# Kernel optimization log

Hardware: AMD Instinct MI355X
Metric: run time of the kernel (lower is better)

The kernel has to match this reference:

```python
import jax, jax.numpy as jnp
import numpy as np

# CLEVR-scale dims
B, N, DF, DE, DV, H, NC, QV, L = 128, 36, 512, 256, 512, 256, 28, 2000, 5


def _lin(key, fan_in, fan_out):
    k1, _ = jax.random.split(key)
    w = jax.random.normal(k1, (fan_in, fan_out), jnp.float32) * np.sqrt(2.0 / fan_in)  # kaiming
    b = jnp.zeros((fan_out,), jnp.float32)
    return w, b


def setup_inputs() -> dict:
    key = jax.random.key(0)
    ks = jax.random.split(key, 12)
    node_feats = jax.random.normal(ks[0], (B, N, DF), jnp.float32)
    edge_feats = jax.random.normal(ks[1], (B, N, N, DE), jnp.float32)
    programs = jax.random.randint(ks[2], (B, L), 0, 10)
    program_inputs = jax.random.randint(ks[3], (B, L), 0, QV)
    W_n1, b_n1 = _lin(ks[4], DF, H)
    W_n2, b_n2 = _lin(ks[5], H, DV)
    W_e1, b_e1 = _lin(ks[6], DE, H)
    W_e2, b_e2 = _lin(ks[7], H, DV)
    W_q, b_q = _lin(ks[8], DV, DV)
    W_c1, b_c1 = _lin(ks[9], DV, H)
    W_c2, b_c2 = _lin(ks[10], H, NC)
    word_emb = jax.random.normal(ks[11], (QV, DV), jnp.float32) / np.sqrt(DV)
    return dict(node_feats=node_feats, edge_feats=edge_feats,
                W_n1=W_n1, b_n1=b_n1, W_n2=W_n2, b_n2=b_n2,
                W_e1=W_e1, b_e1=b_e1, W_e2=W_e2, b_e2=b_e2,
                W_q=W_q, b_q=b_q, W_c1=W_c1, b_c1=b_c1,
                W_c2=W_c2, b_c2=b_c2, word_emb=word_emb,
                programs=programs, program_inputs=program_inputs)


def _mlp(x, W1, b1, W2, b2):
    return jax.nn.relu(x @ W1 + b1) @ W2 + b2


def reference(node_feats, edge_feats, W_n1, b_n1, W_n2, b_n2,
              W_e1, b_e1, W_e2, b_e2, W_q, b_q,
              W_c1, b_c1, W_c2, b_c2, word_emb,
              programs, program_inputs):
    # Fixed representative program (executed in reverse order like the torch code):
    # scene -> filter -> relate -> filter -> query -> classifier
    del programs
    scale = 1.0 / np.sqrt(DV)
    nf = _mlp(node_feats, W_n1, b_n1, W_n2, b_n2)      # [B,N,DV]  map_node_feat_to_v
    ef = _mlp(edge_feats, W_e1, b_e1, W_e2, b_e2)      # [B,N,N,DV] map_edge_feat_to_v
    q = word_emb[program_inputs]                        # [B,L,DV]  word_embedding lookup
    # scene: attention of ones over nodes
    attn = jnp.ones(nf.shape[:2], nf.dtype)             # [B,N]
    # filter (AttentionModule): gate node attention by query-node similarity
    attn = attn * jax.nn.sigmoid(jnp.einsum('bnd,bd->bn', nf, q[:, 3]) * scale)
    # relate (RelateModule): transfer attention along query-weighted edges
    weit = jax.nn.sigmoid(jnp.einsum('bijd,bd->bij', ef, q[:, 2]) * scale)  # [B,N,N]
    attn = jnp.clip(jnp.einsum('bi,bij->bj', attn, weit), 0.0, 1.0)
    # filter again
    attn = attn * jax.nn.sigmoid(jnp.einsum('bnd,bd->bn', nf, q[:, 1]) * scale)
    # query (QueryModule): attention-pooled node feature gated by query, projected
    attn_n = attn / (attn.sum(-1, keepdims=True) + 1e-8)
    pooled = jnp.einsum('bn,bnd->bd', attn_n, nf)        # [B,DV]
    out = jax.nn.relu((pooled * q[:, 0]) @ W_q + b_q)    # [B,DV]
    # classifier
    return jax.nn.relu(out @ W_c1 + b_c1) @ W_c2 + b_c2  # [B,NC]
```

## Files before the change

### kernel.cpp

```cpp
#include <hip/hip_runtime.h>
#include <math.h>

#define BB 128
#define NN 36
#define DF 512
#define DE 256
#define DV 512
#define HH 256
#define NCC 28
#define LQ 5
#define NE 1296
#define SCALE 0.04419417382415922f

#define EDGE_BLOCKS 3456
#define NODE_BLOCKS 288

typedef __bf16 bf16_8 __attribute__((ext_vector_type(8)));
typedef float  f32_4  __attribute__((ext_vector_type(4)));

__device__ __forceinline__ float sigmoidf_(float x){ return 1.0f/(1.0f + expf(-x)); }
__device__ __forceinline__ float reluf_(float x){ return x > 0.f ? x : 0.f; }

__device__ __forceinline__ bf16_8 cvt8(f32_4 f0, f32_4 f1){
    bf16_8 v;
    #pragma unroll
    for (int i=0;i<4;i++){ v[i] = (__bf16)f0[i]; v[i+4] = (__bf16)f1[i]; }
    return v;
}
__device__ __forceinline__ void split8(f32_4 f0, f32_4 f1, bf16_8& h, bf16_8& l){
    #pragma unroll
    for (int i=0;i<4;i++){
        __bf16 hi = (__bf16)f0[i];
        h[i] = hi; l[i] = (__bf16)(f0[i] - (float)hi);
        __bf16 hi2 = (__bf16)f1[i];
        h[i+4] = hi2; l[i+4] = (__bf16)(f1[i] - (float)hi2);
    }
}

__device__ __forceinline__ void async_copy16(const float* g, float* lds_base){
    __builtin_amdgcn_global_load_lds(
        (const __attribute__((address_space(1))) void*)g,
        (__attribute__((address_space(3))) void*)lds_base, 16, 0, 0);
}

#define XROW 516
#define EROW 260

__global__ __launch_bounds__(256) void k_setup(
    const float* __restrict__ W_n1, const float* __restrict__ W_n2,
    const float* __restrict__ W_q,  const float* __restrict__ W_c1,
    const float* __restrict__ W_e1, const float* __restrict__ W_c2,
    const float* __restrict__ word_emb, const int* __restrict__ program_inputs,
    const float* __restrict__ W_e2, const float* __restrict__ b_e2,
    __bf16* __restrict__ Pn1h, __bf16* __restrict__ Pn1l,
    __bf16* __restrict__ Pn2h, __bf16* __restrict__ Pn2l,
    __bf16* __restrict__ Pqh,  __bf16* __restrict__ Pql,
    __bf16* __restrict__ Pc1h, __bf16* __restrict__ Pc1l,
    __bf16* __restrict__ Peh,
    __bf16* __restrict__ Pc2h, __bf16* __restrict__ Pc2l,
    float* __restrict__ qws, float* __restrict__ ve, float* __restrict__ se)
{
    int bid = blockIdx.x;
    if (bid < 356){
        const float* W; __bf16 *Ph, *Pl; int N, base, realN;
        if (bid < 64)       { W=W_n1; Ph=Pn1h; Pl=Pn1l; N=256; base=0;   realN=256; }
        else if (bid < 128) { W=W_n2; Ph=Pn2h; Pl=Pn2l; N=512; base=64;  realN=512; }
        else if (bid < 256) { W=W_q;  Ph=Pqh;  Pl=Pql;  N=512; base=128; realN=512; }
        else if (bid < 320) { W=W_c1; Ph=Pc1h; Pl=Pc1l; N=256; base=256; realN=256; }
        else if (bid < 352) { W=W_e1; Ph=Peh;  Pl=nullptr; N=256; base=320; realN=256; }
        else                { W=W_c2; Ph=Pc2h; Pl=Pc2l; N=32;  base=352; realN=28;  }
        int g = (bid-base)*256 + threadIdx.x;
        int lane = g & 63, slot = g >> 6;
        int NT = N >> 4;
        int nt = slot % NT, kt = slot / NT;
        int krow = kt*32 + (lane>>4)*8, ncol = nt*16 + (lane&15);
        #pragma unroll
        for (int j=0;j<8;j++){
            float w = (ncol < realN) ? W[(size_t)(krow+j)*realN + ncol] : 0.f;
            __bf16 hi = (__bf16)w;
            Ph[(size_t)g*8+j] = hi;
            if (Pl) Pl[(size_t)g*8+j] = (__bf16)(w - (float)hi);
        }
    } else {
        int b = bid - 356, t = threadIdx.x, wv = t>>6, lane = t&63;
        int idx[4];
        #pragma unroll
        for (int k=0;k<4;k++) idx[k] = program_inputs[b*LQ + k];
        #pragma unroll
        for (int k=0;k<4;k++){
            qws[((size_t)(b*4+k))*DV + t]       = word_emb[(size_t)idx[k]*DV + t];
            qws[((size_t)(b*4+k))*DV + t + 256] = word_emb[(size_t)idx[k]*DV + t + 256];
        }
        const float* q2p = word_emb + (size_t)idx[2]*DV + lane*8;
        f32_4 qa = *(const f32_4*)q2p, qb = *(const f32_4*)(q2p+4);
        for (int i=0;i<64;i++){
            int h = wv*64 + i;
            const float* wr = W_e2 + (size_t)h*DV + lane*8;
            f32_4 a = *(const f32_4*)wr, c = *(const f32_4*)(wr+4);
            float p = a[0]*qa[0] + a[1]*qa[1] + a[2]*qa[2] + a[3]*qa[3]
                    + c[0]*qb[0] + c[1]*qb[1] + c[2]*qb[2] + c[3]*qb[3];
            #pragma unroll
            for (int off=32; off; off>>=1) p += __shfl_xor(p, off, 64);
            if (lane==0) ve[b*HH + h] = p;
        }
        float pp = b_e2[t]*word_emb[(size_t)idx[2]*DV + t]
                 + b_e2[t+256]*word_emb[(size_t)idx[2]*DV + t + 256];
        __shared__ float red[4];
        #pragma unroll
        for (int off=32; off; off>>=1) pp += __shfl_down(pp, off, 64);
        if ((t&63)==0) red[t>>6] = pp;
        __syncthreads();
        if (t==0) se[b] = red[0]+red[1]+red[2]+red[3];
    }
}

__device__ __forceinline__ void edge_body(
    int bx, char* smem,
    const float* __restrict__ E, const __bf16* __restrict__ Wp,
    const float* __restrict__ b_e1, const float* __restrict__ ve,
    const float* __restrict__ se, float* __restrict__ weit)
{
    float* es  = (float*)smem;
    float* red = (float*)(smem + 48*EROW*4);
    int b = bx / 27, tile = bx % 27;
    int e0 = tile*48;
    int t = threadIdx.x, wv = t>>6, lane = t&63;
    int m = lane&15, kc = lane>>4;
    const float* Eb = E + ((size_t)b*NE + e0)*DE;

    #pragma unroll
    for (int r=0;r<12;r++){
        int row = wv*12 + r;
        async_copy16(Eb + (size_t)row*DE + lane*4, &es[row*EROW]);
    }
    __syncthreads();

    f32_4 zero = {0.f,0.f,0.f,0.f};
    f32_4 acc[3][4];
    #pragma unroll
    for (int mt=0;mt<3;mt++)
        #pragma unroll
        for (int nt=0;nt<4;nt++) acc[mt][nt] = zero;

    for (int kt=0; kt<8; kt++){
        bf16_8 af[3];
        #pragma unroll
        for (int mt=0;mt<3;mt++){
            const float* ap = &es[(mt*16 + m)*EROW + kt*32 + kc*8];
            af[mt] = cvt8(*(const f32_4*)ap, *(const f32_4*)(ap+4));
        }
        #pragma unroll
        for (int nt=0;nt<4;nt++){
            bf16_8 bfrag = *(const bf16_8*)(Wp + ((size_t)(kt*16 + (wv*4+nt))*64 + lane)*8);
            #pragma unroll
            for (int mt=0;mt<3;mt++)
                acc[mt][nt] = __builtin_amdgcn_mfma_f32_16x16x32_bf16(af[mt], bfrag, acc[mt][nt], 0,0,0);
        }
    }

    float ves[4], be[4];
    #pragma unroll
    for (int nt=0;nt<4;nt++){
        int n = wv*64 + nt*16 + m;
        ves[nt] = ve[b*HH + n];
        be[nt]  = b_e1[n];
    }
    float part[3][4];
    #pragma unroll
    for (int mt=0;mt<3;mt++)
        #pragma unroll
        for (int r=0;r<4;r++){
            float s = 0.f;
            #pragma unroll
            for (int nt=0;nt<4;nt++)
                s = fmaf(reluf_(acc[mt][nt][r] + be[nt]), ves[nt], s);
            part[mt][r] = s;
        }
    #pragma unroll
    for (int off=1; off<16; off<<=1)
        #pragma unroll
        for (int mt=0;mt<3;mt++)
            #pragma unroll
            for (int r=0;r<4;r++)
                part[mt][r] += __shfl_xor(part[mt][r], off, 64);
    if (m==0){
        int g = lane>>4;
        #pragma unroll
        for (int mt=0;mt<3;mt++)
            #pragma unroll
            for (int r=0;r<4;r++)
                red[wv*48 + mt*16 + g*4 + r] = part[mt][r];
    }
    __syncthreads();
    if (t < 48){
        float logit = red[0*48+t]+red[1*48+t]+red[2*48+t]+red[3*48+t] + se[b];
        weit[(size_t)b*NE + e0 + t] = sigmoidf_(logit * SCALE);
    }
}

__device__ __forceinline__ void node_body(
    int nb, char* smem,
    const float* __restrict__ X,
    const __bf16* __restrict__ W1h, const __bf16* __restrict__ W1l,
    const float* __restrict__ b1,
    const __bf16* __restrict__ W2h, const __bf16* __restrict__ W2l,
    const float* __restrict__ b2,
    float* __restrict__ nf)
{
    float* xs  = (float*)smem;
    __bf16* hh = (__bf16*)(smem + 33024);
    __bf16* hl = (__bf16*)(smem + 41216);
    int r0 = nb*16, t = threadIdx.x, wv = t>>6, lane = t&63;
    int m = lane&15, kc = lane>>4;
    int q = lane>>4, c = lane&15;

    #pragma unroll
    for (int r=0;r<4;r++){
        int row = wv*4 + r;
        const float* src = X + (size_t)(r0+row)*DF + lane*4;
        async_copy16(src,       &xs[row*XROW]);
        async_copy16(src + 256, &xs[row*XROW + 256]);
    }
    __syncthreads();

    f32_4 zero = {0.f,0.f,0.f,0.f};
    f32_4 acc1[4];
    #pragma unroll
    for (int nt=0;nt<4;nt++) acc1[nt] = zero;
    for (int kt=0; kt<16; kt++){
        const float* ap = &xs[m*XROW + kt*32 + kc*8];
        f32_4 f0 = *(const f32_4*)ap;
        f32_4 f1 = *(const f32_4*)(ap+4);
        bf16_8 ah, al;
        split8(f0, f1, ah, al);
        #pragma unroll
        for (int nt=0;nt<4;nt++){
            size_t bo = ((size_t)(kt*16 + wv*4+nt)*64 + lane)*8;
            bf16_8 bh = *(const bf16_8*)(W1h + bo);
            bf16_8 bl = *(const bf16_8*)(W1l + bo);
            acc1[nt] = __builtin_amdgcn_mfma_f32_16x16x32_bf16(ah, bh, acc1[nt], 0,0,0);
            acc1[nt] = __builtin_amdgcn_mfma_f32_16x16x32_bf16(al, bh, acc1[nt], 0,0,0);
            acc1[nt] = __builtin_amdgcn_mfma_f32_16x16x32_bf16(ah, bl, acc1[nt], 0,0,0);
        }
    }
    #pragma unroll
    for (int nt=0;nt<4;nt++){
        int col = wv*64 + nt*16 + c;
        float bias = b1[col];
        int kt2 = col>>5, j2 = col&7;
        int lbase = ((col&31)>>3)*16;
        #pragma unroll
        for (int r=0;r<4;r++){
            int row = q*4 + r;
            float v = reluf_(acc1[nt][r] + bias);
            __bf16 hi = (__bf16)v;
            int off = (kt2*64 + lbase + row)*8 + j2;
            hh[off] = hi;
            hl[off] = (__bf16)(v - (float)hi);
        }
    }
    __syncthreads();

    f32_4 acc2[8];
    #pragma unroll
    for (int nt=0;nt<8;nt++) acc2[nt] = zero;
    for (int kt=0; kt<8; kt++){
        bf16_8 ah = *(const bf16_8*)&hh[(kt*64+lane)*8];
        bf16_8 al = *(const bf16_8*)&hl[(kt*64+lane)*8];
        #pragma unroll
        for (int nt=0;nt<8;nt++){
            size_t bo = ((size_t)(kt*32 + wv*8+nt)*64 + lane)*8;
            bf16_8 bh = *(const bf16_8*)(W2h + bo);
            bf16_8 bl = *(const bf16_8*)(W2l + bo);
            acc2[nt] = __builtin_amdgcn_mfma_f32_16x16x32_bf16(ah, bh, acc2[nt], 0,0,0);
            acc2[nt] = __builtin_amdgcn_mfma_f32_16x16x32_bf16(al, bh, acc2[nt], 0,0,0);
            acc2[nt] = __builtin_amdgcn_mfma_f32_16x16x32_bf16(ah, bl, acc2[nt], 0,0,0);
        }
    }
    #pragma unroll
    for (int nt=0;nt<8;nt++){
        int col = wv*128 + nt*16 + c;
        float bias = b2[col];
        #pragma unroll
        for (int r=0;r<4;r++){
            int row = q*4 + r;
            nf[(size_t)(r0+row)*DV + col] = acc2[nt][r] + bias;
        }
    }
}

__global__ __launch_bounds__(256) void k_main(
    const float* __restrict__ E, const __bf16* __restrict__ Wp,
    const float* __restrict__ b_e1, const float* __restrict__ ve,
    const float* __restrict__ se, float* __restrict__ weit,
    const float* __restrict__ X,
    const __bf16* __restrict__ W1h, const __bf16* __restrict__ W1l,
    const float* __restrict__ b1,
    const __bf16* __restrict__ W2h, const __bf16* __restrict__ W2l,
    const float* __restrict__ b2,
    float* __restrict__ nf)
{
    __shared__ __align__(16) char smem[50688];
    int bx = blockIdx.x;
    if (bx < EDGE_BLOCKS)
        edge_body(bx, smem, E, Wp, b_e1, ve, se, weit);
    else
        node_body(bx - EDGE_BLOCKS, smem, X, W1h, W1l, b1, W2h, W2l, b2, nf);
}

__global__ __launch_bounds__(256) void k_attn(
    const float* __restrict__ nf, const float* __restrict__ qws,
    const float* __restrict__ weit, float* __restrict__ xws)
{
    int b = blockIdx.x, t = threadIdx.x;
    int wv = t>>6, lane = t&63;
    __shared__ float a1[NN], a2[NN], a3[NN];
    __shared__ float denom;
    const float* nfb = nf + (size_t)b*NN*DV;
    const float* q0 = qws + ((size_t)(b*4+0))*DV;
    const float* q1 = qws + ((size_t)(b*4+1))*DV;
    const float* q3 = qws + ((size_t)(b*4+3))*DV;

    #pragma unroll
    for (int i=wv; i<NN; i+=4){
        const float* row = nfb + (size_t)i*DV + lane*8;
        const float* qq  = q3 + lane*8;
        f32_4 x0 = *(const f32_4*)row, x1 = *(const f32_4*)(row+4);
        f32_4 y0 = *(const f32_4*)qq,  y1 = *(const f32_4*)(qq+4);
        float p = x0[0]*y0[0] + x0[1]*y0[1] + x0[2]*y0[2] + x0[3]*y0[3]
                + x1[0]*y1[0] + x1[1]*y1[1] + x1[2]*y1[2] + x1[3]*y1[3];
        #pragma unroll
        for (int off=32; off; off>>=1) p += __shfl_xor(p, off, 64);
        if (lane==0) a1[i] = sigmoidf_(p*SCALE);
    }
    __syncthreads();
    if (t < NN){
        const float* wrow = weit + (size_t)b*NE;
        float s = 0.f;
        #pragma unroll
        for (int i=0;i<NN;i++) s = fmaf(a1[i], wrow[i*NN + t], s);
        a2[t] = fminf(fmaxf(s, 0.f), 1.f);
    }
    __syncthreads();
    #pragma unroll
    for (int i=wv; i<NN; i+=4){
        const float* row = nfb + (size_t)i*DV + lane*8;
        const float* qq  = q1 + lane*8;
        f32_4 x0 = *(const f32_4*)row, x1 = *(const f32_4*)(row+4);
        f32_4 y0 = *(const f32_4*)qq,  y1 = *(const f32_4*)(qq+4);
        float p = x0[0]*y0[0] + x0[1]*y0[1] + x0[2]*y0[2] + x0[3]*y0[3]
                + x1[0]*y1[0] + x1[1]*y1[1] + x1[2]*y1[2] + x1[3]*y1[3];
        #pragma unroll
        for (int off=32; off; off>>=1) p += __shfl_xor(p, off, 64);
        if (lane==0) a3[i] = a2[i]*sigmoidf_(p*SCALE);
    }
    __syncthreads();
    if (t==0){
        float s = 0.f;
        for (int i=0;i<NN;i++) s += a3[i];
        denom = 1.f/(s + 1e-8f);
    }
    __syncthreads();
    float p0=0.f, p1=0.f;
    #pragma unroll
    for (int i=0;i<NN;i++){
        float a = a3[i]*denom;
        p0 = fmaf(a, nfb[(size_t)i*DV + t], p0);
        p1 = fmaf(a, nfb[(size_t)i*DV + t + 256], p1);
    }
    xws[(size_t)b*DV + t]       = p0*q0[t];
    xws[(size_t)b*DV + t + 256] = p1*q0[t+256];
}

__global__ __launch_bounds__(256) void k_head(
    const float* __restrict__ xws,
    const __bf16* __restrict__ Wqh, const __bf16* __restrict__ Wql,
    const float* __restrict__ b_q,
    const __bf16* __restrict__ Wc1h, const __bf16* __restrict__ Wc1l,
    const float* __restrict__ b_c1,
    const __bf16* __restrict__ Pc2h, const __bf16* __restrict__ Pc2l,
    const float* __restrict__ b_c2,
    float* __restrict__ out)
{
    __shared__ __align__(16) char smem[49408];
    float* xs   = (float*)smem;
    __bf16* oh  = (__bf16*)smem;
    __bf16* ol  = (__bf16*)(smem + 16384);
    __bf16* hfh = (__bf16*)(smem + 33024);
    __bf16* hfl = (__bf16*)(smem + 41216);

    int r0 = blockIdx.x*16, t = threadIdx.x, wv = t>>6, lane = t&63;
    int m = lane&15, kc = lane>>4;
    int q = lane>>4, c = lane&15;
    f32_4 zero = {0.f,0.f,0.f,0.f};

    #pragma unroll
    for (int r=0;r<4;r++){
        int row = wv*4 + r;
        const float* src = xws + (size_t)(r0+row)*DV + lane*4;
        async_copy16(src,       &xs[row*XROW]);
        async_copy16(src + 256, &xs[row*XROW + 256]);
    }
    __syncthreads();

    f32_4 acc[8];
    #pragma unroll
    for (int nt=0;nt<8;nt++) acc[nt] = zero;
    for (int kt=0; kt<16; kt++){
        const float* ap = &xs[m*XROW + kt*32 + kc*8];
        f32_4 f0 = *(const f32_4*)ap;
        f32_4 f1 = *(const f32_4*)(ap+4);
        bf16_8 ah, al;
        split8(f0, f1, ah, al);
        #pragma unroll
        for (int nt=0;nt<8;nt++){
            size_t bo = ((size_t)(kt*32 + wv*8+nt)*64 + lane)*8;
            bf16_8 bh = *(const bf16_8*)(Wqh + bo);
            bf16_8 bl = *(const bf16_8*)(Wql + bo);
            acc[nt] = __builtin_amdgcn_mfma_f32_16x16x32_bf16(ah, bh, acc[nt], 0,0,0);
            acc[nt] = __builtin_amdgcn_mfma_f32_16x16x32_bf16(al, bh, acc[nt], 0,0,0);
            acc[nt] = __builtin_amdgcn_mfma_f32_16x16x32_bf16(ah, bl, acc[nt], 0,0,0);
        }
    }
    __syncthreads();
    #pragma unroll
    for (int nt=0;nt<8;nt++){
        int col = wv*128 + nt*16 + c;
        float bias = b_q[col];
        int kt2 = col>>5, j2 = col&7;
        int lbase = ((col&31)>>3)*16;
        #pragma unroll
        for (int r=0;r<4;r++){
            int row = q*4 + r;
            float v = reluf_(acc[nt][r] + bias);
            __bf16 hi = (__bf16)v;
            int off = (kt2*64 + lbase + row)*8 + j2;
            oh[off] = hi;
            ol[off] = (__bf16)(v - (float)hi);
        }
    }
    __syncthreads();

    f32_4 acc2[4];
    #pragma unroll
    for (int nt=0;nt<4;nt++) acc2[nt] = zero;
    for (int kt=0; kt<16; kt++){
        bf16_8 ah = *(const bf16_8*)&oh[(kt*64+lane)*8];
        bf16_8 al = *(const bf16_8*)&ol[(kt*64+lane)*8];
        #pragma unroll
        for (int nt=0;nt<4;nt++){
            size_t bo = ((size_t)(kt*16 + wv*4+nt)*64 + lane)*8;
            bf16_8 bh = *(const bf16_8*)(Wc1h + bo);
            bf16_8 bl = *(const bf16_8*)(Wc1l + bo);
            acc2[nt] = __builtin_amdgcn_mfma_f32_16x16x32_bf16(ah, bh, acc2[nt], 0,0,0);
            acc2[nt] = __builtin_amdgcn_mfma_f32_16x16x32_bf16(al, bh, acc2[nt], 0,0,0);
            acc2[nt] = __builtin_amdgcn_mfma_f32_16x16x32_bf16(ah, bl, acc2[nt], 0,0,0);
        }
    }
    #pragma unroll
    for (int nt=0;nt<4;nt++){
        int col = wv*64 + nt*16 + c;
        float bias = b_c1[col];
        int kt2 = col>>5, j2 = col&7;
        int lbase = ((col&31)>>3)*16;
        #pragma unroll
        for (int r=0;r<4;r++){
            int row = q*4 + r;
            float v = reluf_(acc2[nt][r] + bias);
            __bf16 hi = (__bf16)v;
            int off = (kt2*64 + lbase + row)*8 + j2;
            hfh[off] = hi;
            hfl[off] = (__bf16)(v - (float)hi);
        }
    }
    __syncthreads();

    if (wv < 2){
        f32_4 acc3 = zero;
        for (int kt=0; kt<8; kt++){
            bf16_8 ah = *(const bf16_8*)&hfh[(kt*64+lane)*8];
            bf16_8 al = *(const bf16_8*)&hfl[(kt*64+lane)*8];
            size_t bo = ((size_t)(kt*2 + wv)*64 + lane)*8;
            bf16_8 bh = *(const bf16_8*)(Pc2h + bo);
            bf16_8 bl = *(const bf16_8*)(Pc2l + bo);
            acc3 = __builtin_amdgcn_mfma_f32_16x16x32_bf16(ah, bh, acc3, 0,0,0);
            acc3 = __builtin_amdgcn_mfma_f32_16x16x32_bf16(al, bh, acc3, 0,0,0);
            acc3 = __builtin_amdgcn_mfma_f32_16x16x32_bf16(ah, bl, acc3, 0,0,0);
        }
        int col = wv*16 + c;
        if (col < NCC){
            float bias = b_c2[col];
            #pragma unroll
            for (int r=0;r<4;r++){
                int row = q*4 + r;
                out[(size_t)(r0+row)*NCC + col] = acc3[r] + bias;
            }
        }
    }
}

extern "C" void kernel_launch(void* const* d_in, const int* in_sizes, int n_in,
                              void* d_out, int out_size, void* d_ws, size_t ws_size,
                              hipStream_t stream)
{
    const float* node_feats = (const float*)d_in[0];
    const float* edge_feats = (const float*)d_in[1];
    const float* W_n1 = (const float*)d_in[2];
    const float* b_n1 = (const float*)d_in[3];
    const float* W_n2 = (const float*)d_in[4];
    const float* b_n2 = (const float*)d_in[5];
    const float* W_e1 = (const float*)d_in[6];
    const float* b_e1 = (const float*)d_in[7];
    const float* W_e2 = (const float*)d_in[8];
    const float* b_e2 = (const float*)d_in[9];
    const float* W_q  = (const float*)d_in[10];
    const float* b_q  = (const float*)d_in[11];
    const float* W_c1 = (const float*)d_in[12];
    const float* b_c1 = (const float*)d_in[13];
    const float* W_c2 = (const float*)d_in[14];
    const float* b_c2 = (const float*)d_in[15];
    const float* word_emb = (const float*)d_in[16];
    const int* program_inputs = (const int*)d_in[18];

    char* ws = (char*)d_ws;
    float* qws  = (float*)ws; ws += (size_t)BB*4*DV*4;
    float* ve   = (float*)ws; ws += (size_t)BB*HH*4;
    float* se   = (float*)ws; ws += 512;
    float* xws  = (float*)ws; ws += (size_t)BB*DV*4;
    __bf16* Pn1h = (__bf16*)ws; ws += (size_t)DF*HH*2;
    __bf16* Pn1l = (__bf16*)ws; ws += (size_t)DF*HH*2;
    __bf16* Pn2h = (__bf16*)ws; ws += (size_t)HH*DV*2;
    __bf16* Pn2l = (__bf16*)ws; ws += (size_t)HH*DV*2;
    __bf16* Pqh  = (__bf16*)ws; ws += (size_t)DV*DV*2;
    __bf16* Pql  = (__bf16*)ws; ws += (size_t)DV*DV*2;
    __bf16* Pc1h = (__bf16*)ws; ws += (size_t)DV*HH*2;
    __bf16* Pc1l = (__bf16*)ws; ws += (size_t)DV*HH*2;
    __bf16* Peh  = (__bf16*)ws; ws += (size_t)DE*HH*2;
    __bf16* Pc2h = (__bf16*)ws; ws += (size_t)HH*32*2;
    __bf16* Pc2l = (__bf16*)ws; ws += (size_t)HH*32*2;
    float* nf   = (float*)ws; ws += (size_t)BB*NN*DV*4;
    float* weit = (float*)ws; ws += (size_t)BB*NE*4;

    k_setup<<<484, 256, 0, stream>>>(W_n1, W_n2, W_q, W_c1, W_e1, W_c2,
                                     word_emb, program_inputs, W_e2, b_e2,
                                     Pn1h, Pn1l, Pn2h, Pn2l, Pqh, Pql, Pc1h, Pc1l,
                                     Peh, Pc2h, Pc2l, qws, ve, se);
    k_main<<<EDGE_BLOCKS + NODE_BLOCKS, 256, 0, stream>>>(
        edge_feats, Peh, b_e1, ve, se, weit,
        node_feats, Pn1h, Pn1l, b_n1, Pn2h, Pn2l, b_n2, nf);
    k_attn<<<BB, 256, 0, stream>>>(nf, qws, weit, xws);
    k_head<<<BB/16, 256, 0, stream>>>(xws, Pqh, Pql, b_q, Pc1h, Pc1l, b_c1,
                                      Pc2h, Pc2l, b_c2, (float*)d_out);
}
```

Baseline: 447.7 us.

## Split edge MLP into persistent kernel with LDS-resident weights and register streaming

The edge MLP moves out of the fused edge/node kernel into a persistent kernel with 256 blocks of 1024 threads. Each block loads the whole bf16 W_e1 (128KB) into LDS once, and each wave loops over 16-edge tiles. Edge features stream straight from global memory into registers with one-step prefetch, instead of being staged through LDS. The node MLP becomes its own kernel, which serializes the node and edge work. The edge loop also risks limited occupancy, since only one block fits per CU, and leaves less latency hiding for the roughly 340MB edge-feature read.

```diff
diff --git a/kernel.cpp b/kernel.cpp
--- a/kernel.cpp
+++ b/kernel.cpp
@@ -12,8 +12,10 @@
 #define NE 1296
 #define SCALE 0.04419417382415922f
 
-#define EDGE_BLOCKS 3456
 #define NODE_BLOCKS 288
+#define ETILES 10368
+#define EBLOCKS 256
+#define EWAVES 4096
 
 typedef __bf16 bf16_8 __attribute__((ext_vector_type(8)));
 typedef float  f32_4  __attribute__((ext_vector_type(4)));
@@ -44,7 +46,6 @@
 }
 
 #define XROW 516
-#define EROW 260
 
 __global__ __launch_bounds__(256) void k_setup(
     const float* __restrict__ W_n1, const float* __restrict__ W_n2,
@@ -114,90 +115,6 @@
     }
 }
 
-__device__ __forceinline__ void edge_body(
-    int bx, char* smem,
-    const float* __restrict__ E, const __bf16* __restrict__ Wp,
-    const float* __restrict__ b_e1, const float* __restrict__ ve,
-    const float* __restrict__ se, float* __restrict__ weit)
-{
-    float* es  = (float*)smem;
-    float* red = (float*)(smem + 48*EROW*4);
-    int b = bx / 27, tile = bx % 27;
-    int e0 = tile*48;
-    int t = threadIdx.x, wv = t>>6, lane = t&63;
-    int m = lane&15, kc = lane>>4;
-    const float* Eb = E + ((size_t)b*NE + e0)*DE;
-
-    #pragma unroll
-    for (int r=0;r<12;r++){
-        int row = wv*12 + r;
-        async_copy16(Eb + (size_t)row*DE + lane*4, &es[row*EROW]);
-    }
-    __syncthreads();
-
-    f32_4 zero = {0.f,0.f,0.f,0.f};
-    f32_4 acc[3][4];
-    #pragma unroll
-    for (int mt=0;mt<3;mt++)
-        #pragma unroll
-        for (int nt=0;nt<4;nt++) acc[mt][nt] = zero;
-
-    for (int kt=0; kt<8; kt++){
-        bf16_8 af[3];
-        #pragma unroll
-        for (int mt=0;mt<3;mt++){
-            const float* ap = &es[(mt*16 + m)*EROW + kt*32 + kc*8];
-            af[mt] = cvt8(*(const f32_4*)ap, *(const f32_4*)(ap+4));
-        }
-        #pragma unroll
-        for (int nt=0;nt<4;nt++){
-            bf16_8 bfrag = *(const bf16_8*)(Wp + ((size_t)(kt*16 + (wv*4+nt))*64 + lane)*8);
-            #pragma unroll
-            for (int mt=0;mt<3;mt++)
-                acc[mt][nt] = __builtin_amdgcn_mfma_f32_16x16x32_bf16(af[mt], bfrag, acc[mt][nt], 0,0,0);
-        }
-    }
-
-    float ves[4], be[4];
-    #pragma unroll
-    for (int nt=0;nt<4;nt++){
-        int n = wv*64 + nt*16 + m;
-        ves[nt] = ve[b*HH + n];
-        be[nt]  = b_e1[n];
-    }
-    float part[3][4];
-    #pragma unroll
-    for (int mt=0;mt<3;mt++)
-        #pragma unroll
-        for (int r=0;r<4;r++){
-            float s = 0.f;
-            #pragma unroll
-            for (int nt=0;nt<4;nt++)
-                s = fmaf(reluf_(acc[mt][nt][r] + be[nt]), ves[nt], s);
-            part[mt][r] = s;
-        }
-    #pragma unroll
-    for (int off=1; off<16; off<<=1)
-        #pragma unroll
-        for (int mt=0;mt<3;mt++)
-            #pragma unroll
-            for (int r=0;r<4;r++)
-                part[mt][r] += __shfl_xor(part[mt][r], off, 64);
-    if (m==0){
-        int g = lane>>4;
-        #pragma unroll
-        for (int mt=0;mt<3;mt++)
-            #pragma unroll
-            for (int r=0;r<4;r++)
-                red[wv*48 + mt*16 + g*4 + r] = part[mt][r];
-    }
-    __syncthreads();
-    if (t < 48){
-        float logit = red[0*48+t]+red[1*48+t]+red[2*48+t]+red[3*48+t] + se[b];
-        weit[(size_t)b*NE + e0 + t] = sigmoidf_(logit * SCALE);
-    }
-}
-
 __device__ __forceinline__ void node_body(
     int nb, char* smem,
     const float* __restrict__ X,
@@ -289,10 +206,7 @@
     }
 }
 
-__global__ __launch_bounds__(256) void k_main(
-    const float* __restrict__ E, const __bf16* __restrict__ Wp,
-    const float* __restrict__ b_e1, const float* __restrict__ ve,
-    const float* __restrict__ se, float* __restrict__ weit,
+__global__ __launch_bounds__(256) void k_node(
     const float* __restrict__ X,
     const __bf16* __restrict__ W1h, const __bf16* __restrict__ W1l,
     const float* __restrict__ b1,
@@ -300,12 +214,82 @@
     const float* __restrict__ b2,
     float* __restrict__ nf)
 {
-    __shared__ __align__(16) char smem[50688];
-    int bx = blockIdx.x;
-    if (bx < EDGE_BLOCKS)
-        edge_body(bx, smem, E, Wp, b_e1, ve, se, weit);
-    else
-        node_body(bx - EDGE_BLOCKS, smem, X, W1h, W1l, b1, W2h, W2l, b2, nf);
+    __shared__ __align__(16) char smem[49408];
+    node_body(blockIdx.x, smem, X, W1h, W1l, b1, W2h, W2l, b2, nf);
+}
+
+__global__ __launch_bounds__(1024) void k_edge(
+    const float* __restrict__ E, const __bf16* __restrict__ Wp,
+    const float* __restrict__ b_e1, const float* __restrict__ ve,
+    const float* __restrict__ se, float* __restrict__ weit)
+{
+    __shared__ __align__(16) __bf16 wlds[DE*HH];
+    int t = threadIdx.x, wv = t>>6, lane = t&63;
+    int m = lane&15, kc = lane>>4;
+
+    #pragma unroll
+    for (int i=0;i<8;i++){
+        int off = (wv*8 + i) << 10;
+        async_copy16((const float*)((const char*)Wp + off) + lane*4,
+                     (float*)((char*)wlds + off));
+    }
+    __syncthreads();
+
+    for (int tile = blockIdx.x*16 + wv; tile < ETILES; tile += EWAVES){
+        int b = tile/81, tt = tile - b*81;
+        int e0 = tt*16;
+        const float* Ea = E + ((size_t)b*NE + e0 + m)*DE + kc*8;
+
+        f32_4 zero = {0.f,0.f,0.f,0.f};
+        f32_4 acc[16];
+        #pragma unroll
+        for (int nt=0;nt<16;nt++) acc[nt] = zero;
+
+        f32_4 c0 = *(const f32_4*)Ea;
+        f32_4 c1 = *(const f32_4*)(Ea+4);
+        #pragma unroll
+        for (int kt=0;kt<8;kt++){
+            f32_4 n0, n1;
+            if (kt < 7){
+                n0 = *(const f32_4*)(Ea + (kt+1)*32);
+                n1 = *(const f32_4*)(Ea + (kt+1)*32 + 4);
+            }
+            bf16_8 af = cvt8(c0, c1);
+            #pragma unroll
+            for (int nt=0;nt<16;nt++){
+                bf16_8 bfrag = *(const bf16_8*)&wlds[((size_t)(kt*16+nt)*64 + lane)*8];
+                acc[nt] = __builtin_amdgcn_mfma_f32_16x16x32_bf16(af, bfrag, acc[nt], 0,0,0);
+            }
+            c0 = n0; c1 = n1;
+        }
+
+        float s0=0.f, s1=0.f, s2=0.f, s3=0.f;
+        #pragma unroll
+        for (int nt=0;nt<16;nt++){
+            float bev = b_e1[nt*16 + m];
+            float vev = ve[b*HH + nt*16 + m];
+            s0 = fmaf(reluf_(acc[nt][0] + bev), vev, s0);
+            s1 = fmaf(reluf_(acc[nt][1] + bev), vev, s1);
+            s2 = fmaf(reluf_(acc[nt][2] + bev), vev, s2);
+            s3 = fmaf(reluf_(acc[nt][3] + bev), vev, s3);
+        }
+        #pragma unroll
+        for (int off=1; off<16; off<<=1){
+            s0 += __shfl_xor(s0, off, 64);
+            s1 += __shfl_xor(s1, off, 64);
+            s2 += __shfl_xor(s2, off, 64);
+            s3 += __shfl_xor(s3, off, 64);
+        }
+        float seb = se[b];
+        if (m == 0){
+            f32_4 o;
+            o[0] = sigmoidf_((s0 + seb)*SCALE);
+            o[1] = sigmoidf_((s1 + seb)*SCALE);
+            o[2] = sigmoidf_((s2 + seb)*SCALE);
+            o[3] = sigmoidf_((s3 + seb)*SCALE);
+            *(f32_4*)&weit[(size_t)b*NE + e0 + kc*4] = o;
+        }
+    }
 }
 
 __global__ __launch_bounds__(256) void k_attn(
@@ -545,9 +529,10 @@
                                      word_emb, program_inputs, W_e2, b_e2,
                                      Pn1h, Pn1l, Pn2h, Pn2l, Pqh, Pql, Pc1h, Pc1l,
                                      Peh, Pc2h, Pc2l, qws, ve, se);
-    k_main<<<EDGE_BLOCKS + NODE_BLOCKS, 256, 0, stream>>>(
-        edge_feats, Peh, b_e1, ve, se, weit,
+    k_node<<<NODE_BLOCKS, 256, 0, stream>>>(
         node_feats, Pn1h, Pn1l, b_n1, Pn2h, Pn2l, b_n2, nf);
+    k_edge<<<EBLOCKS, 1024, 0, stream>>>(
+        edge_feats, Peh, b_e1, ve, se, weit);
     k_attn<<<BB, 256, 0, stream>>>(nf, qws, weit, xws);
     k_head<<<BB/16, 256, 0, stream>>>(xws, Pqh, Pql, b_q, Pc1h, Pc1l, b_c1,
                                       Pc2h, Pc2l, b_c2, (float*)d_out);
```

Result: slower. 901.7 us (+101.4%).
